# Kernel tuning notes

Measured on AMD Instinct MI355X. Metric: run time of the kernel, lower is better.

## Reference

```python
import jax, jax.numpy as jnp
import numpy as np

# pywt db4 decomposition low-pass filter (dec_lo), length 8
_DEC_LO = np.array([-0.010597401784997278, 0.032883011666982945,
                    0.030841381835986965, -0.18703481171888114,
                    -0.02798376941698385, 0.6308807679295904,
                    0.7148465705525415, 0.23037781330885523], dtype=np.float32)
FLEN = 8
LEVELS = 9            # pywt.dwt_max_level(4096, 8) == 9
# pywt computes a convolution with dec_lo == correlation with reversed dec_lo
_KERNEL = jnp.asarray(_DEC_LO[::-1].copy()).reshape(1, 1, FLEN)


def _dwt_lo(a):
    """One DWT level (approximation branch only), pywt 'symmetric' mode.
    Output length = floor((n + FLEN - 1) / 2), matching pywt.dwt."""
    pad = [(0, 0)] * (a.ndim - 1) + [(FLEN - 1, FLEN - 1)]
    p = jnp.pad(a, pad, mode='symmetric')[..., 1:]  # correlation starts at offset 1
    bflat = int(np.prod(a.shape[:-1]))
    y = jax.lax.conv_general_dilated(p.reshape(bflat, 1, -1), _KERNEL,
                                     window_strides=(2,), padding='VALID')
    return y.reshape(a.shape[:-1] + (y.shape[-1],))


def wavedec_approx(x):
    a = x
    for _ in range(LEVELS):  # fixed small level count, not a data-dim loop
        a = _dwt_lo(a)
    return a  # [..., 14]


def setup_inputs() -> dict:
    key = jax.random.key(0)
    k1, k2, k3 = jax.random.split(key, 3)
    x = jax.random.normal(k1, (32, 512, 4096), dtype=jnp.float32)
    W = jax.random.normal(k2, (14, 14), dtype=jnp.float32) * (1.0 / np.sqrt(14.0).astype(np.float32))
    b = jax.random.normal(k3, (14,), dtype=jnp.float32) * 0.01
    return {"x": x, "W": W, "b": b}


def reference(x, W, b):
    # original detaches x before the wavelet transform
    approx = wavedec_approx(jax.lax.stop_gradient(x))          # [B, S, 14]
    aug = jnp.einsum('bsf,of->bso', approx, W) + b             # Linear(14, 14)
    return jnp.concatenate([x, aug], axis=-1)                  # [B, S, 4096 + 14]
```

## Files before the change

### kernel.cpp

```cpp
#include <hip/hip_runtime.h>


#define ROWS 16384
#define N0   4096
#define OUTW 4110

typedef __attribute__((ext_vector_type(8))) short bf16x8;
typedef __attribute__((ext_vector_type(4))) float f32x4;

__device__ __constant__ float c_dlo[8] = {
    -0.010597401784997278f,  0.032883011666982945f,
     0.030841381835986965f, -0.18703481171888114f,
    -0.02798376941698385f,   0.6308807679295904f,
     0.7148465705525415f,    0.23037781330885523f};

__device__ __forceinline__ unsigned short f2bf(float f) {
    unsigned u = __float_as_uint(f);
    return (unsigned short)((u + 0x7FFFu + ((u >> 16) & 1u)) >> 16);
}

__device__ __forceinline__ float adj_contrib(const float* __restrict__ g,
                                             int t, int nout) {
    int i0 = t >> 1;        if (i0 < 0) i0 = 0;
    int i1 = (t + 6) >> 1;  if (i1 > nout - 1) i1 = nout - 1;
    float acc = 0.f;
    for (int i = i0; i <= i1; ++i)
        acc = fmaf(g[i], c_dlo[2 * i + 1 - t], acc);
    return acc;
}

__global__ __launch_bounds__(256) void build_cm_kernel(
    const float* __restrict__ W, unsigned short* __restrict__ cmT)
{
    __shared__ float A[4096];
    __shared__ float B[2051];
    const int o = blockIdx.x, tid = threadIdx.x;
    if (tid < 14) B[tid] = (o < 14) ? W[o * 14 + tid] : 0.f;
    __syncthreads();
    const int ns[10] = {14, 22, 38, 70, 134, 262, 518, 1029, 2051, 4096};
    float* g = B;
    float* h = A;
    for (int lev = 1; lev <= 9; ++lev) {
        const int n = ns[lev], nout = ns[lev - 1];
        const int s2 = 2 * (n - nout);
        for (int s = tid; s < n; s += 256) {
            float v = adj_contrib(g, s, nout);
            if (s <= 5)  v += adj_contrib(g, -1 - s, nout);
            if (s >= s2) v += adj_contrib(g, 2 * n - 1 - s, nout);
            h[s] = v;
        }
        __syncthreads();
        float* t2 = g; g = h; h = t2;
    }
    for (int c = tid; c < 4096; c += 256)
        cmT[o * 4096 + c] = f2bf(g[c]);
}

__global__ __launch_bounds__(256) void wavelet_aug_mfma(
    const float* __restrict__ x, const unsigned short* __restrict__ cmT,
    const float* __restrict__ b, float* __restrict__ out)
{
    __shared__ __align__(16) unsigned short xt[32][136];
    __shared__ float parts[4][64][4];

    const int tid  = threadIdx.x;
    const int wave = tid >> 6;
    const int lane = tid & 63;
    const int r    = lane & 15;
    const int g    = lane >> 4;
    const int row0 = blockIdx.x << 4;

    const unsigned short* cr = cmT + r * N0;
    f32x4 acc = {0.f, 0.f, 0.f, 0.f};

    #pragma unroll 2
    for (int it = 0; it < 16; ++it) {
        const int kb = it << 8;

        const int kbw = kb + (wave << 6) + (g << 3);
        const bf16x8 bv0 = *reinterpret_cast<const bf16x8*>(cr + kbw);
        const bf16x8 bv1 = *reinterpret_cast<const bf16x8*>(cr + kbw + 32);

        float4 a[4];
        #pragma unroll
        for (int i = 0; i < 4; ++i) {
            const int rr = (i << 2) + wave;
            a[i] = *reinterpret_cast<const float4*>(
                x + (size_t)(row0 + rr) * N0 + kb + (lane << 2));
        }
        #pragma unroll
        for (int i = 0; i < 4; ++i) {
            const int rr = (i << 2) + wave;
            float* orow = out + (size_t)(row0 + rr) * OUTW + kb + (lane << 2);
            reinterpret_cast<float2*>(orow)[0] = make_float2(a[i].x, a[i].y);
            reinterpret_cast<float2*>(orow)[1] = make_float2(a[i].z, a[i].w);
            ushort4 u;
            u.x = f2bf(a[i].x); u.y = f2bf(a[i].y);
            u.z = f2bf(a[i].z); u.w = f2bf(a[i].w);
            *reinterpret_cast<ushort4*>(
                &xt[lane >> 1][(rr << 3) + ((lane & 1) << 2)]) = u;
        }
        __syncthreads();

        #pragma unroll
        for (int t = 0; t < 2; ++t) {
            const int ch = (wave << 3) + (t << 2) + g;
            const bf16x8 av =
                *reinterpret_cast<const bf16x8*>(&xt[ch][r << 3]);
            acc = __builtin_amdgcn_mfma_f32_16x16x32_bf16(
                av, t ? bv1 : bv0, acc, 0, 0, 0);
        }
        __syncthreads();
    }

    parts[wave][lane][0] = acc[0];
    parts[wave][lane][1] = acc[1];
    parts[wave][lane][2] = acc[2];
    parts[wave][lane][3] = acc[3];
    __syncthreads();

    if (tid < 64) {
        const float4 p0 = *reinterpret_cast<const float4*>(parts[0][tid]);
        const float4 p1 = *reinterpret_cast<const float4*>(parts[1][tid]);
        const float4 p2 = *reinterpret_cast<const float4*>(parts[2][tid]);
        const float4 p3 = *reinterpret_cast<const float4*>(parts[3][tid]);
        const int col   = tid & 15;
        const int rbase = (tid >> 4) << 2;
        if (col < 14) {
            const float bb = b[col];
            out[(size_t)(row0 + rbase + 0) * OUTW + N0 + col] = p0.x + p1.x + p2.x + p3.x + bb;
            out[(size_t)(row0 + rbase + 1) * OUTW + N0 + col] = p0.y + p1.y + p2.y + p3.y + bb;
            out[(size_t)(row0 + rbase + 2) * OUTW + N0 + col] = p0.z + p1.z + p2.z + p3.z + bb;
            out[(size_t)(row0 + rbase + 3) * OUTW + N0 + col] = p0.w + p1.w + p2.w + p3.w + bb;
        }
    }
}

extern "C" void kernel_launch(void* const* d_in, const int* in_sizes, int n_in,
                              void* d_out, int out_size, void* d_ws, size_t ws_size,
                              hipStream_t stream) {
    const float* x = (const float*)d_in[0];
    const float* W = (const float*)d_in[1];
    const float* b = (const float*)d_in[2];
    float* out = (float*)d_out;
    unsigned short* cmT = (unsigned short*)d_ws;

    build_cm_kernel<<<16, 256, 0, stream>>>(W, cmT);
    wavelet_aug_mfma<<<ROWS / 16, 256, 0, stream>>>(x, cmT, b, out);
}
```

Before: 154.1 us.

## Give each wave its own 16 rows with register prefetch and no block barriers

Each wave now owns 16 full rows and keeps its partial products in a wave-private LDS tile, so the block-wide __syncthreads and the cross-wave reduction go away. The next 256-column tile is loaded into registers while the current one is written out and fed to MFMA. The coefficient matrix is stored pre-swizzled so each lane reads its B fragments with one contiguous vector load, and the grid shrinks to 64 rows per block. The price is much higher register pressure from 32 float4 buffers, which may lower occupancy, and fewer blocks in flight.

Result: slower. 158.1 us (+2.6%).

```diff
diff --git a/kernel.cpp b/kernel.cpp
--- a/kernel.cpp
+++ b/kernel.cpp
@@ -4,6 +4,9 @@
 #define ROWS 16384
 #define N0   4096
 #define OUTW 4110
+#define BK   256
+#define ITERS (N0 / BK)
+#define LROW 264
 
 typedef __attribute__((ext_vector_type(8))) short bf16x8;
 typedef __attribute__((ext_vector_type(4))) float f32x4;
@@ -30,7 +33,7 @@
 }
 
 __global__ __launch_bounds__(256) void build_cm_kernel(
-    const float* __restrict__ W, unsigned short* __restrict__ cmT)
+    const float* __restrict__ W, unsigned short* __restrict__ cmB)
 {
     __shared__ float A[4096];
     __shared__ float B[2051];
@@ -52,86 +55,89 @@
         __syncthreads();
         float* t2 = g; g = h; h = t2;
     }
-    for (int c = tid; c < 4096; c += 256)
-        cmT[o * 4096 + c] = f2bf(g[c]);
+    for (int c = tid; c < 4096; c += 256) {
+        const int S = c >> 5, gg = (c >> 3) & 3, j = c & 7;
+        cmB[(((S << 6) + (gg << 4) + o) << 3) + j] = f2bf(g[c]);
+    }
 }
 
 __global__ __launch_bounds__(256) void wavelet_aug_mfma(
-    const float* __restrict__ x, const unsigned short* __restrict__ cmT,
+    const float* __restrict__ x, const unsigned short* __restrict__ cmB,
     const float* __restrict__ b, float* __restrict__ out)
 {
-    __shared__ __align__(16) unsigned short xt[32][136];
-    __shared__ float parts[4][64][4];
+    __shared__ __align__(16) unsigned short xt[4][16][LROW];
 
     const int tid  = threadIdx.x;
     const int wave = tid >> 6;
     const int lane = tid & 63;
     const int r    = lane & 15;
     const int g    = lane >> 4;
-    const int row0 = blockIdx.x << 4;
+    const int wr0  = (blockIdx.x << 6) + (wave << 4);
 
-    const unsigned short* cr = cmT + r * N0;
+    const float* xw  = x   + (size_t)wr0 * N0 + (lane << 2);
+    float*       ow  = out + (size_t)wr0 * OUTW + (lane << 2);
+    const bf16x8* cb = reinterpret_cast<const bf16x8*>(cmB);
+    unsigned short* lds = &xt[wave][0][0];
+
     f32x4 acc = {0.f, 0.f, 0.f, 0.f};
 
-    #pragma unroll 2
-    for (int it = 0; it < 16; ++it) {
+    float4 tile[16];
+    #pragma unroll
+    for (int i = 0; i < 16; ++i)
+        tile[i] = *reinterpret_cast<const float4*>(xw + (size_t)i * N0);
+
+    #pragma unroll 1
+    for (int it = 0; it < ITERS; ++it) {
         const int kb = it << 8;
 
-        const int kbw = kb + (wave << 6) + (g << 3);
-        const bf16x8 bv0 = *reinterpret_cast<const bf16x8*>(cr + kbw);
-        const bf16x8 bv1 = *reinterpret_cast<const bf16x8*>(cr + kbw + 32);
-
-        float4 a[4];
+        float4 nxt[16];
+        if (it < ITERS - 1) {
+            #pragma unroll
+            for (int i = 0; i < 16; ++i)
+                nxt[i] = *reinterpret_cast<const float4*>(
+                    xw + (size_t)i * N0 + kb + BK);
+        }
+        bf16x8 bv[8];
         #pragma unroll
-        for (int i = 0; i < 4; ++i) {
-            const int rr = (i << 2) + wave;
-            a[i] = *reinterpret_cast<const float4*>(
-                x + (size_t)(row0 + rr) * N0 + kb + (lane << 2));
-        }
-        #pragma unroll
-        for (int i = 0; i < 4; ++i) {
-            const int rr = (i << 2) + wave;
-            float* orow = out + (size_t)(row0 + rr) * OUTW + kb + (lane << 2);
-            reinterpret_cast<float2*>(orow)[0] = make_float2(a[i].x, a[i].y);
-            reinterpret_cast<float2*>(orow)[1] = make_float2(a[i].z, a[i].w);
-            ushort4 u;
-            u.x = f2bf(a[i].x); u.y = f2bf(a[i].y);
-            u.z = f2bf(a[i].z); u.w = f2bf(a[i].w);
-            *reinterpret_cast<ushort4*>(
-                &xt[lane >> 1][(rr << 3) + ((lane & 1) << 2)]) = u;
-        }
-        __syncthreads();
+        for (int s = 0; s < 8; ++s)
+            bv[s] = cb[(((it << 3) + s) << 6) + lane];
 
         #pragma unroll
-        for (int t = 0; t < 2; ++t) {
-            const int ch = (wave << 3) + (t << 2) + g;
-            const bf16x8 av =
-                *reinterpret_cast<const bf16x8*>(&xt[ch][r << 3]);
-            acc = __builtin_amdgcn_mfma_f32_16x16x32_bf16(
-                av, t ? bv1 : bv0, acc, 0, 0, 0);
+        for (int i = 0; i < 16; ++i) {
+            const float4 a = tile[i];
+            float* orow = ow + (size_t)i * OUTW + kb;
+            if (i & 1) {
+                reinterpret_cast<float2*>(orow)[0] = make_float2(a.x, a.y);
+                reinterpret_cast<float2*>(orow)[1] = make_float2(a.z, a.w);
+            } else {
+                *reinterpret_cast<float4*>(orow) = a;
+            }
+            ushort4 u;
+            u.x = f2bf(a.x); u.y = f2bf(a.y); u.z = f2bf(a.z); u.w = f2bf(a.w);
+            *reinterpret_cast<ushort4*>(lds + i * LROW + (lane << 2)) = u;
         }
-        __syncthreads();
+
+        asm volatile("s_waitcnt lgkmcnt(0)" ::: "memory");
+        __builtin_amdgcn_sched_barrier(0);
+
+        #pragma unroll
+        for (int s = 0; s < 8; ++s) {
+            const bf16x8 av = *reinterpret_cast<const bf16x8*>(
+                lds + r * LROW + (s << 5) + (g << 3));
+            acc = __builtin_amdgcn_mfma_f32_16x16x32_bf16(av, bv[s], acc, 0, 0, 0);
+        }
+
+        #pragma unroll
+        for (int i = 0; i < 16; ++i) tile[i] = nxt[i];
     }
 
-    parts[wave][lane][0] = acc[0];
-    parts[wave][lane][1] = acc[1];
-    parts[wave][lane][2] = acc[2];
-    parts[wave][lane][3] = acc[3];
-    __syncthreads();
-
-    if (tid < 64) {
-        const float4 p0 = *reinterpret_cast<const float4*>(parts[0][tid]);
-        const float4 p1 = *reinterpret_cast<const float4*>(parts[1][tid]);
-        const float4 p2 = *reinterpret_cast<const float4*>(parts[2][tid]);
-        const float4 p3 = *reinterpret_cast<const float4*>(parts[3][tid]);
-        const int col   = tid & 15;
-        const int rbase = (tid >> 4) << 2;
-        if (col < 14) {
-            const float bb = b[col];
-            out[(size_t)(row0 + rbase + 0) * OUTW + N0 + col] = p0.x + p1.x + p2.x + p3.x + bb;
-            out[(size_t)(row0 + rbase + 1) * OUTW + N0 + col] = p0.y + p1.y + p2.y + p3.y + bb;
-            out[(size_t)(row0 + rbase + 2) * OUTW + N0 + col] = p0.z + p1.z + p2.z + p3.z + bb;
-            out[(size_t)(row0 + rbase + 3) * OUTW + N0 + col] = p0.w + p1.w + p2.w + p3.w + bb;
+    const int col = lane & 15;
+    if (col < 14) {
+        const float bb = b[col];
+        #pragma unroll
+        for (int j = 0; j < 4; ++j) {
+            const int row = wr0 + ((lane >> 4) << 2) + j;
+            out[(size_t)row * OUTW + N0 + col] = acc[j] + bb;
         }
     }
 }
@@ -143,8 +149,8 @@
     const float* W = (const float*)d_in[1];
     const float* b = (const float*)d_in[2];
     float* out = (float*)d_out;
-    unsigned short* cmT = (unsigned short*)d_ws;
+    unsigned short* cmB = (unsigned short*)d_ws;
 
-    build_cm_kernel<<<16, 256, 0, stream>>>(W, cmT);
-    wavelet_aug_mfma<<<ROWS / 16, 256, 0, stream>>>(x, cmT, b, out);
+    build_cm_kernel<<<16, 256, 0, stream>>>(W, cmB);
+    wavelet_aug_mfma<<<ROWS / 64, 256, 0, stream>>>(x, cmB, b, out);
 }
```
